# Optimization experiments

Hardware: AMD Instinct MI355X
Metric: run time of the kernel (lower is better)

The kernel has to match this reference:

```python
import jax, jax.numpy as jnp
import numpy as np

EPS = 1e-5

def group_norm(x, num_groups, eps=EPS):
    # x: [B, C, H, W]; no affine (matches F.group_norm with weight=None)
    B, C, H, W = x.shape
    xg = x.reshape(B, num_groups, (C // num_groups) * H * W)
    mean = jnp.mean(xg, axis=-1, keepdims=True)
    var = jnp.var(xg, axis=-1, keepdims=True)
    xg = (xg - mean) * jax.lax.rsqrt(var + eps)
    return xg.reshape(B, C, H, W)

def setup_inputs() -> dict:
    key = jax.random.key(0)
    ks = jax.random.split(key, 5)
    B, C, H, W = 32, 256, 32, 32
    # kaiming-uniform-ish scale for linear weights
    bound = 1.0 / np.sqrt(C)
    x = jax.random.normal(ks[0], (B, C, H, W), dtype=jnp.float32)
    WQ = jax.random.uniform(ks[1], (C, C), jnp.float32, -bound, bound)
    WK = jax.random.uniform(ks[2], (C, C), jnp.float32, -bound, bound)
    WV = jax.random.uniform(ks[3], (C, C), jnp.float32, -bound, bound)
    Wo = jax.random.uniform(ks[4], (C, C), jnp.float32, -bound, bound)
    z = jnp.zeros((C,), jnp.float32)
    return {"x": x, "WQ": WQ, "bQ": z, "WK": WK, "bK": z,
            "WV": WV, "bV": z, "Wo": Wo, "bo": z}

def reference(x, WQ, bQ, WK, bK, WV, bV, Wo, bo):
    B, C, H, W = x.shape
    G = min(32, C)
    h = group_norm(x, G)                      # [B,C,H,W]
    h = h.reshape(B, C, H * W).transpose(0, 2, 1)  # [B, S, C], S = H*W
    q = h @ WQ + bQ
    k = h @ WK + bK
    v = h @ WV + bV
    scale = C ** (-0.5)
    attn = jnp.einsum('bsc,btc->bst', q, k) * scale   # [B,S,S]
    attn = jax.nn.softmax(attn, axis=-1)
    o = jnp.einsum('bst,btc->bsc', attn, v)           # [B,S,C]
    o = o @ Wo + bo                                   # output Nin while in [B,S,C]
    o = o.transpose(0, 2, 1).reshape(B, C, H, W)
    return x + o
```

## Files before the change

### kernel.cpp

```cpp
#include <hip/hip_runtime.h>
#include <stdint.h>

#define BB  32
#define CC  256
#define SS  1024
#define GG  32
#define GCH 8
#define EPS 1e-5f

typedef __attribute__((ext_vector_type(8))) short short8;
typedef __attribute__((ext_vector_type(4))) float f32x4;
typedef __attribute__((ext_vector_type(16))) float f32x16;
typedef unsigned short ushort;

__device__ __forceinline__ float bf2f(ushort u){
  union { unsigned int i; float f; } v; v.i = ((unsigned int)u) << 16; return v.f;
}
__device__ __forceinline__ ushort f2bf(float f){
  union { float f; unsigned int i; } v; v.f = f;
  unsigned int r = v.i + 0x7FFFu + ((v.i >> 16) & 1u);
  return (ushort)(r >> 16);
}

typedef __attribute__((address_space(3))) unsigned int lds_uint;
typedef const __attribute__((address_space(1))) unsigned int glob_uint;
__device__ __forceinline__ void ld_lds16(const void* g, void* l){
  __builtin_amdgcn_global_load_lds((glob_uint*)g, (lds_uint*)l, 16, 0, 0);
}

__global__ __launch_bounds__(256) void sniff_k(const unsigned int* __restrict__ xw,
                                               int* __restrict__ flag)
{
  const int tid = threadIdx.x;
  unsigned int w = xw[tid];
  ushort lo = (ushort)(w & 0xFFFFu);
  int e = (lo >> 7) & 0xFF;
  int ok = (lo == 0 || (e >= 100 && e <= 130)) ? 1 : 0;
  __shared__ int cnt;
  if (tid == 0) cnt = 0;
  __syncthreads();
  atomicAdd(&cnt, ok);
  __syncthreads();
  if (tid == 0) *flag = (cnt > 192) ? 1 : 0;
}

__global__ __launch_bounds__(256) void convert_pre(
    const void* w0, const void* w1, const void* w2, const void* w3,
    const void* b0, const void* b1, const void* b2, const void* b3,
    ushort* __restrict__ WT, float* __restrict__ biasF,
    const int* __restrict__ flag)
{
  const int f = *flag;
  const int z = blockIdx.z;
  const float scl = (z == 0) ? 0.0625f : 1.0f;
  const void* wsel = z==0?w0:z==1?w1:z==2?w2:w3;
  ushort* dst = WT + (long long)z * 65536;
  __shared__ ushort t[64][65];
  const int tid = threadIdx.x;
  const int tx = tid & 63, ty = tid >> 6;
  const int r0 = blockIdx.x * 64, c0 = blockIdx.y * 64;
  for (int j = 0; j < 64; j += 4){
    const int idx = (r0+ty+j)*256 + c0+tx;
    float v = f ? bf2f(((const ushort*)wsel)[idx]) : ((const float*)wsel)[idx];
    t[ty+j][tx] = f2bf(v * scl);
  }
  __syncthreads();
  for (int j = 0; j < 64; j += 4) dst[(c0+ty+j)*256 + r0+tx] = t[tx][ty+j];
  if (blockIdx.x == 0 && blockIdx.y == 0){
    const void* bsel = z==0?b0:z==1?b1:z==2?b2:b3;
    float bv = f ? bf2f(((const ushort*)bsel)[tid]) : ((const float*)bsel)[tid];
    biasF[z*256 + tid] = bv * scl;
  }
}

__global__ __launch_bounds__(256) void gn_stats(const void* __restrict__ x,
                                                float* __restrict__ stats,
                                                const int* __restrict__ flag)
{
  const int f = *flag;
  const int g = blockIdx.x, b = blockIdx.y;
  const int tid = threadIdx.x;
  const long long base = ((long long)b * CC + g * GCH) * SS;
  float sum = 0.f, ss = 0.f;
  if (f){
    const ushort* xg = (const ushort*)x + base;
    #pragma unroll
    for (int j = 0; j < 4; j++){
      uint4 u = *(const uint4*)(xg + (j*256 + tid)*8);
      const ushort* e = (const ushort*)&u;
      #pragma unroll
      for (int i = 0; i < 8; i++){ float v = bf2f(e[i]); sum += v; ss += v*v; }
    }
  } else {
    const float* xg = (const float*)x + base;
    #pragma unroll
    for (int j = 0; j < 8; j++){
      float4 v4 = *(const float4*)(xg + (j*256 + tid)*4);
      sum += v4.x+v4.y+v4.z+v4.w;
      ss  += v4.x*v4.x+v4.y*v4.y+v4.z*v4.z+v4.w*v4.w;
    }
  }
  __shared__ float red[8];
  const int lane = tid & 63, w = tid >> 6;
  #pragma unroll
  for (int o = 32; o > 0; o >>= 1){
    sum += __shfl_down(sum, o);
    ss  += __shfl_down(ss, o);
  }
  if (lane == 0){ red[w] = sum; red[4+w] = ss; }
  __syncthreads();
  if (tid == 0){
    float s1 = red[0]+red[1]+red[2]+red[3];
    float s2 = red[4]+red[5]+red[6]+red[7];
    float mean = s1 / (float)(GCH*SS);
    float var  = s2 / (float)(GCH*SS) - mean*mean;
    const int idx = b*GG + g;
    stats[idx*2]   = mean;
    stats[idx*2+1] = rsqrtf(var + EPS);
  }
}

__global__ __launch_bounds__(256) void gn_norm(const void* __restrict__ x,
                                               ushort* __restrict__ h,
                                               const float* __restrict__ stats,
                                               const int* __restrict__ flag)
{
  const int f = *flag;
  const int c0 = blockIdx.x * 64, s0 = blockIdx.y * 64, b = blockIdx.z;
  const int tid = threadIdx.x;
  __shared__ ushort T[64][72];
  const int row = tid >> 2;
  const int qr  = tid & 3;
  const int g = (c0 + row) >> 3;
  const float mean = stats[(b*GG + g)*2];
  const float rstd = stats[(b*GG + g)*2 + 1];
  const long long xrow = ((long long)b * CC + c0 + row) * SS + s0;
  if (f){
    const ushort* xr = (const ushort*)x + xrow;
    #pragma unroll
    for (int j = 0; j < 2; j++){
      const int col = qr*16 + j*8;
      uint4 u = *(const uint4*)(xr + col);
      const ushort* e = (const ushort*)&u;
      #pragma unroll
      for (int i = 0; i < 8; i++) T[row][col+i] = f2bf((bf2f(e[i]) - mean) * rstd);
    }
  } else {
    const float* xr = (const float*)x + xrow;
    #pragma unroll
    for (int j = 0; j < 4; j++){
      const int col = qr*16 + j*4;
      float4 v4 = *(const float4*)(xr + col);
      T[row][col+0] = f2bf((v4.x - mean) * rstd);
      T[row][col+1] = f2bf((v4.y - mean) * rstd);
      T[row][col+2] = f2bf((v4.z - mean) * rstd);
      T[row][col+3] = f2bf((v4.w - mean) * rstd);
    }
  }
  __syncthreads();
  #pragma unroll
  for (int pass = 0; pass < 2; pass++){
    const int sr = pass*32 + (tid >> 3);
    const int cl = (tid & 7) * 8;
    ushort tmp[8];
    #pragma unroll
    for (int e = 0; e < 8; e++) tmp[e] = T[cl+e][sr];
    *(uint4*)(&h[((long long)b * SS + s0 + sr) * CC + c0 + cl]) = *(const uint4*)tmp;
  }
}

template<int MODE>
__global__ __launch_bounds__(256) void gemm128(
    const ushort* __restrict__ A,
    const ushort* __restrict__ BT,
    ushort* __restrict__ Cmat,
    int lda, int ldb, int ldc, int K,
    long long sA, long long sB, long long sC,
    const float* __restrict__ biasF,
    const void* __restrict__ xres,
    void* __restrict__ outp,
    ushort* __restrict__ vTp,
    long long xoff,
    const int* __restrict__ flag)
{
  extern __shared__ __attribute__((aligned(16))) ushort smem[];
  ushort* As = smem;
  ushort* Bs = smem + 5120;
  const int tid  = threadIdx.x;
  const int lane = tid & 63;
  const int w    = tid >> 6;
  const int wr   = w >> 1, wc = w & 1;
  const int bz   = blockIdx.z;
  const int m0 = blockIdx.x * 128;
  const int n0 = blockIdx.y * 128;

  const int srow  = tid >> 1;
  const int shalf = (tid & 1) * 16;

  f32x4 acc[4][4] = {};

  const ushort* Ablk = A + (long long)bz * sA + (long long)(m0 + srow) * lda + shalf;
  const ushort* Bblk = BT + (long long)bz * sB + (long long)(n0 + srow) * ldb + shalf;
  ushort* asw = &As[srow * 40 + shalf];
  ushort* bsw = &Bs[srow * 40 + shalf];

  const int koff = 8 * (lane >> 4);
  const int rr   = lane & 15;

  for (int k0 = 0; k0 < K; k0 += 32){
    uint4 va0 = *(const uint4*)(Ablk + k0);
    uint4 va1 = *(const uint4*)(Ablk + k0 + 8);
    uint4 vb0 = *(const uint4*)(Bblk + k0);
    uint4 vb1 = *(const uint4*)(Bblk + k0 + 8);
    *(uint4*)(asw)     = va0;
    *(uint4*)(asw + 8) = va1;
    *(uint4*)(bsw)     = vb0;
    *(uint4*)(bsw + 8) = vb1;
    __syncthreads();
    short8 af[4], bfr[4];
    #pragma unroll
    for (int mf = 0; mf < 4; mf++)
      af[mf] = *(const short8*)(&As[(wr*64 + mf*16 + rr) * 40 + koff]);
    #pragma unroll
    for (int nf = 0; nf < 4; nf++)
      bfr[nf] = *(const short8*)(&Bs[(wc*64 + nf*16 + rr) * 40 + koff]);
    #pragma unroll
    for (int mf = 0; mf < 4; mf++)
      #pragma unroll
      for (int nf = 0; nf < 4; nf++)
        acc[mf][nf] = __builtin_amdgcn_mfma_f32_16x16x32_bf16(af[mf], bfr[nf], acc[mf][nf], 0, 0, 0);
    __syncthreads();
  }

  const int rb = 4 * (lane >> 4);
  if (MODE == 0){
    if (bz < 2){
      ushort* Co = Cmat + (long long)bz * sC;
      #pragma unroll
      for (int mf = 0; mf < 4; mf++){
        #pragma unroll
        for (int nf = 0; nf < 4; nf++){
          const int col = n0 + wc*64 + nf*16 + rr;
          const float badd = biasF[bz*256 + col];
          #pragma unroll
          for (int r = 0; r < 4; r++){
            const int row = m0 + wr*64 + mf*16 + rb + r;
            Co[(long long)row * ldc + col] = f2bf(acc[mf][nf][r] + badd);
          }
        }
      }
    } else {
      #pragma unroll
      for (int mf = 0; mf < 4; mf++){
        #pragma unroll
        for (int nf = 0; nf < 4; nf++){
          const int col = n0 + wc*64 + nf*16 + rr;
          const float badd = biasF[512 + col];
          #pragma unroll
          for (int r = 0; r < 4; r++){
            const int row = m0 + wr*64 + mf*16 + rb + r;
            const int bL = row >> 10, s = row & 1023;
            vTp[((long long)bL * CC + col) * SS + s] = f2bf(acc[mf][nf][r] + badd);
          }
        }
      }
    }
  } else {
    const int bL = m0 >> 10;
    const int s0 = m0 & 1023;
    #pragma unroll
    for (int mf = 0; mf < 4; mf++){
      #pragma unroll
      for (int nf = 0; nf < 4; nf++){
        const int colL = wc*64 + nf*16 + rr;
        const float badd = biasF[768 + n0 + colL];
        #pragma unroll
        for (int r = 0; r < 4; r++){
          const int rowL = wr*64 + mf*16 + rb + r;
          smem[colL * 128 + rowL] = f2bf(acc[mf][nf][r] + badd);
        }
      }
    }
    __syncthreads();
    const int f = *flag;
    for (int i = tid; i < 2048; i += 256){
      const int colL = i >> 4;
      const int rowL = (i & 15) * 8;
      const long long oi = xoff + ((long long)bL * CC + n0 + colL) * SS + s0 + rowL;
      const ushort* pu = &smem[colL * 128 + rowL];
      if (f){
        const ushort* xu = (const ushort*)xres + oi;
        ushort* ou = (ushort*)outp + oi;
        ushort tmp[8];
        #pragma unroll
        for (int e = 0; e < 8; e++) tmp[e] = f2bf(bf2f(xu[e]) + bf2f(pu[e]));
        *(uint4*)ou = *(const uint4*)tmp;
      } else {
        const float* xf = (const float*)xres + oi;
        float* of = (float*)outp + oi;
        float4 a0 = *(const float4*)xf;
        float4 a1 = *(const float4*)(xf + 4);
        float4 r0, r1;
        r0.x = a0.x + bf2f(pu[0]); r0.y = a0.y + bf2f(pu[1]);
        r0.z = a0.z + bf2f(pu[2]); r0.w = a0.w + bf2f(pu[3]);
        r1.x = a1.x + bf2f(pu[4]); r1.y = a1.y + bf2f(pu[5]);
        r1.z = a1.z + bf2f(pu[6]); r1.w = a1.w + bf2f(pu[7]);
        *(float4*)of = r0;
        *(float4*)(of + 4) = r1;
      }
    }
  }
}

__global__ __launch_bounds__(512, 1) void attn_fused(
    const ushort* __restrict__ q, const ushort* __restrict__ k,
    const ushort* __restrict__ vT, ushort* __restrict__ oC)
{
  __shared__ ushort Kb[2][64 * 256];
  __shared__ ushort Vb[2][256 * 64];
  const int tid = threadIdx.x, lane = tid & 63, w = tid >> 6;
  const int l31 = lane & 31, hi2 = lane >> 5;
  const int qg = w & 3, ch = w >> 2;
  const int b = blockIdx.x, qt = blockIdx.y;

  const char* kgB = (const char*)(k + (long long)b * SS * CC);
  const char* vgB = (const char*)(vT + (long long)b * CC * SS);
  const int qrow = qt*128 + qg*32 + l31;
  const ushort* qgp = q + ((long long)b * SS + qrow) * CC + hi2*8;
  ushort* ogq = oC + ((long long)b * SS + qrow) * CC + ch*128;

  short8 qf[16];
  #pragma unroll
  for (int kk = 0; kk < 16; kk++)
    qf[kk] = *(const short8*)(qgp + kk*16);

  f32x16 Oa[4] = {};
  float mrow = -1e30f, lrow = 0.0f;

  #define STAGE(buf, t0)                                                        \
  {                                                                             \
    _Pragma("unroll")                                                           \
    for (int j = 0; j < 4; j++){                                                \
      const int ck = j*8 + w;                                                   \
      const int tr = ck*2 + (lane >> 5);                                        \
      const int xb = ((lane & 31) * 16) ^ ((tr & 31) << 4);                     \
      ld_lds16(kgB + (long long)((t0) + tr) * 512 + xb, &Kb[buf][ck * 512]);    \
    }                                                                           \
    _Pragma("unroll")                                                           \
    for (int j = 0; j < 4; j++){                                                \
      const int ck = j*8 + w;                                                   \
      const int cr = ck*8 + (lane >> 3);                                        \
      const int yb = ((lane & 7) * 16) ^ ((cr & 7) << 4);                       \
      ld_lds16(vgB + (long long)cr * 2048 + (t0)*2 + yb, &Vb[buf][ck * 512]);   \
    }                                                                           \
  }

  STAGE(0, 0);
  asm volatile("s_waitcnt vmcnt(0)" ::: "memory");
  __builtin_amdgcn_sched_barrier(0);
  __syncthreads();

  const int coff = hi2 * 16;
  const int kswz = l31 << 4;

  for (int t = 0; t < 16; t++){
    const int cur = t & 1;
    if (t < 15) STAGE(cur ^ 1, (t+1)*64);

    f32x16 Sa0 = {}, Sa1 = {};
    __builtin_amdgcn_s_setprio(1);
    #pragma unroll
    for (int kk = 0; kk < 16; kk++){
      const int off = kk*32 + coff;
      short8 ka0 = *(const short8*)((const char*)&Kb[cur][0] + l31*512 + (off ^ kswz));
      short8 ka1 = *(const short8*)((const char*)&Kb[cur][0] + (32 + l31)*512 + (off ^ kswz));
      Sa0 = __builtin_amdgcn_mfma_f32_32x32x16_bf16(ka0, qf[kk], Sa0, 0, 0, 0);
      Sa1 = __builtin_amdgcn_mfma_f32_32x32x16_bf16(ka1, qf[kk], Sa1, 0, 0, 0);
    }
    __builtin_amdgcn_s_setprio(0);

    float mx = Sa0[0];
    #pragma unroll
    for (int r = 1; r < 16; r++) mx = fmaxf(mx, Sa0[r]);
    #pragma unroll
    for (int r = 0; r < 16; r++) mx = fmaxf(mx, Sa1[r]);
    mx = fmaxf(mx, __shfl_xor(mx, 32));
    if (!__all(mx <= mrow)){
      const float mn = fmaxf(mrow, mx);
      const float sc = __expf(mrow - mn);
      mrow = mn;
      lrow *= sc;
      #pragma unroll
      for (int nf = 0; nf < 4; nf++)
        #pragma unroll
        for (int r = 0; r < 16; r++) Oa[nf][r] *= sc;
    }
    float rs = 0.0f;
    #pragma unroll
    for (int r = 0; r < 16; r++){
      Sa0[r] = __expf(Sa0[r] - mrow); rs += Sa0[r];
      Sa1[r] = __expf(Sa1[r] - mrow); rs += Sa1[r];
    }
    rs += __shfl_xor(rs, 32);
    lrow += rs;

    __builtin_amdgcn_s_setprio(1);
    #pragma unroll
    for (int g = 0; g < 4; g++){
      float pv[8];
      #pragma unroll
      for (int j = 0; j < 8; j++)
        pv[j] = (g < 2) ? Sa0[(g & 1)*8 + j] : Sa1[(g & 1)*8 + j];
      unsigned int b0 = ((unsigned int)f2bf(pv[1]) << 16) | f2bf(pv[0]);
      unsigned int b1 = ((unsigned int)f2bf(pv[3]) << 16) | f2bf(pv[2]);
      unsigned int b2 = ((unsigned int)f2bf(pv[5]) << 16) | f2bf(pv[4]);
      unsigned int b3 = ((unsigned int)f2bf(pv[7]) << 16) | f2bf(pv[6]);
      unsigned int s0 = (unsigned int)__shfl_xor((int)b0, 32);
      unsigned int s1 = (unsigned int)__shfl_xor((int)b1, 32);
      unsigned int s2 = (unsigned int)__shfl_xor((int)b2, 32);
      unsigned int s3 = (unsigned int)__shfl_xor((int)b3, 32);
      union { uint4 u; short8 s; } pw;
      pw.u.x = hi2 ? s2 : b0;
      pw.u.y = hi2 ? s3 : b1;
      pw.u.z = hi2 ? b2 : s0;
      pw.u.w = hi2 ? b3 : s1;
      const short8 pb = pw.s;
      const int voff = g*32 + coff;
      #pragma unroll
      for (int nf = 0; nf < 4; nf++){
        const int c = ch*128 + nf*32 + l31;
        short8 va = *(const short8*)((const char*)&Vb[cur][0] + c*128 + (voff ^ ((c & 7) << 4)));
        Oa[nf] = __builtin_amdgcn_mfma_f32_32x32x16_bf16(va, pb, Oa[nf], 0, 0, 0);
      }
    }
    __builtin_amdgcn_s_setprio(0);

    asm volatile("s_waitcnt vmcnt(0)" ::: "memory");
    __builtin_amdgcn_sched_barrier(0);
    __syncthreads();
  }
  #undef STAGE

  const float inv = 1.0f / lrow;
  #pragma unroll
  for (int nf = 0; nf < 4; nf++){
    #pragma unroll
    for (int g = 0; g < 4; g++){
      ushort t4[4];
      #pragma unroll
      for (int j = 0; j < 4; j++) t4[j] = f2bf(Oa[nf][g*4 + j] * inv);
      *(uint2*)(ogq + nf*32 + g*8 + hi2*4) = *(const uint2*)t4;
    }
  }
}

extern "C" void kernel_launch(void* const* d_in, const int* in_sizes, int n_in,
                              void* d_out, int out_size, void* d_ws, size_t ws_size,
                              hipStream_t stream)
{
  (void)in_sizes; (void)n_in; (void)out_size;
  const void* x  = d_in[0];
  const void* WQ = d_in[1];
  const void* bQ = d_in[2];
  const void* WK = d_in[3];
  const void* bK = d_in[4];
  const void* WV = d_in[5];
  const void* bV = d_in[6];
  const void* Wo = d_in[7];
  const void* bo = d_in[8];

  const long long NE  = (long long)BB * SS * CC;
  const long long SC  = (long long)SS * CC;

  uint8_t* base = (uint8_t*)d_ws;
  int* flag          = (int*)base;
  float* biasF       = (float*)(base + 256);
  float* stats       = (float*)(base + 256 + 4096);
  ushort* WT         = (ushort*)(base + 256 + 4096 + 8192);
  ushort* h          = WT + 4 * 65536;

  const long long fixedB = 256 + 4096 + 8192 + 4LL*65536*2 + NE*2;
  int CB = 1;
  for (int c = 32; c >= 1; c >>= 1){
    if (fixedB + 4LL * c * SC * 2 <= (long long)ws_size){ CB = c; break; }
  }

  ushort* q  = h + NE;
  ushort* k  = q + (long long)CB * SC;
  ushort* vT = k + (long long)CB * SC;
  ushort* oC = vT + (long long)CB * SC;

  dim3 blk(256);
  const size_t shmem = 32768;

  sniff_k<<<1, blk, 0, stream>>>((const unsigned int*)x, flag);
  convert_pre<<<dim3(4, 4, 4), blk, 0, stream>>>(WQ, WK, WV, Wo, bQ, bK, bV, bo, WT, biasF, flag);
  gn_stats<<<dim3(GG, BB), blk, 0, stream>>>(x, stats, flag);
  gn_norm<<<dim3(4, 16, BB), blk, 0, stream>>>(x, h, stats, flag);

  for (int c0 = 0; c0 < BB; c0 += CB){
    const ushort* hC = h + (long long)c0 * SC;
    gemm128<0><<<dim3(CB*8, 2, 3), blk, shmem, stream>>>(
        hC, WT, q, CC, CC, CC, CC,
        0LL, 65536LL, (long long)CB * SC,
        biasF, nullptr, nullptr, vT, 0LL, flag);
    attn_fused<<<dim3(CB, 8), dim3(512), 0, stream>>>(q, k, vT, oC);
    gemm128<3><<<dim3(CB*8, 2, 1), blk, shmem, stream>>>(
        oC, WT + 3*65536, nullptr, CC, CC, SS, CC,
        0LL, 0LL, 0LL,
        biasF, x, d_out, nullptr, (long long)c0 * SC, flag);
  }
}
```

Before: 163.0 us.

## Use exp2 softmax with folded log2e, lazy rescale, packed bf16 converts, new V swizzle

Folds log2(e) into the Q weight scale so the softmax can use the native exp2 instruction instead of __expf. It also skips rescaling the running max unless the new max exceeds the old by more than 8, and replaces manual bf16 rounding with the hardware v_cvt_pk_bf16_f32 instruction. Separately, it changes the V tile LDS layout and swizzle, likely to cut bank conflicts on the PV MFMA operand loads. The lazy rescale trades some headroom against overflow of the exponentials for fewer rescale passes over the accumulators.

```diff
diff --git a/kernel.cpp b/kernel.cpp
--- a/kernel.cpp
+++ b/kernel.cpp
@@ -20,6 +20,11 @@
   union { float f; unsigned int i; } v; v.f = f;
   unsigned int r = v.i + 0x7FFFu + ((v.i >> 16) & 1u);
   return (ushort)(r >> 16);
+}
+__device__ __forceinline__ unsigned int cvt_pk_bf16(float lo, float hi){
+  unsigned int r;
+  asm("v_cvt_pk_bf16_f32 %0, %1, %2" : "=v"(r) : "v"(lo), "v"(hi));
+  return r;
 }
 
 typedef __attribute__((address_space(3))) unsigned int lds_uint;
@@ -52,7 +57,7 @@
 {
   const int f = *flag;
   const int z = blockIdx.z;
-  const float scl = (z == 0) ? 0.0625f : 1.0f;
+  const float scl = (z == 0) ? 0.0901684400557f : 1.0f;
   const void* wsel = z==0?w0:z==1?w1:z==2?w2:w3;
   ushort* dst = WT + (long long)z * 65536;
   __shared__ ushort t[64][65];
@@ -349,9 +354,11 @@
     _Pragma("unroll")                                                           \
     for (int j = 0; j < 4; j++){                                                \
       const int ck = j*8 + w;                                                   \
-      const int cr = ck*8 + (lane >> 3);                                        \
-      const int yb = ((lane & 7) * 16) ^ ((cr & 7) << 4);                       \
-      ld_lds16(vgB + (long long)cr * 2048 + (t0)*2 + yb, &Vb[buf][ck * 512]);   \
+      const int vr = ck*2 + (lane >> 5);                                        \
+      const int u  = (lane & 31) ^ ((vr & 7) << 2);                             \
+      const int vc = vr*4 + (u & 3);                                            \
+      const int tb = (u >> 2) * 16;                                             \
+      ld_lds16(vgB + (long long)vc * 2048 + (t0)*2 + tb, &Vb[buf][ck * 512]);   \
     }                                                                           \
   }
 
@@ -385,9 +392,9 @@
     #pragma unroll
     for (int r = 0; r < 16; r++) mx = fmaxf(mx, Sa1[r]);
     mx = fmaxf(mx, __shfl_xor(mx, 32));
-    if (!__all(mx <= mrow)){
+    if (!__all(mx <= mrow + 8.0f)){
       const float mn = fmaxf(mrow, mx);
-      const float sc = __expf(mrow - mn);
+      const float sc = __builtin_amdgcn_exp2f(mrow - mn);
       mrow = mn;
       lrow *= sc;
       #pragma unroll
@@ -398,8 +405,8 @@
     float rs = 0.0f;
     #pragma unroll
     for (int r = 0; r < 16; r++){
-      Sa0[r] = __expf(Sa0[r] - mrow); rs += Sa0[r];
-      Sa1[r] = __expf(Sa1[r] - mrow); rs += Sa1[r];
+      Sa0[r] = __builtin_amdgcn_exp2f(Sa0[r] - mrow); rs += Sa0[r];
+      Sa1[r] = __builtin_amdgcn_exp2f(Sa1[r] - mrow); rs += Sa1[r];
     }
     rs += __shfl_xor(rs, 32);
     lrow += rs;
@@ -407,14 +414,18 @@
     __builtin_amdgcn_s_setprio(1);
     #pragma unroll
     for (int g = 0; g < 4; g++){
-      float pv[8];
-      #pragma unroll
-      for (int j = 0; j < 8; j++)
-        pv[j] = (g < 2) ? Sa0[(g & 1)*8 + j] : Sa1[(g & 1)*8 + j];
-      unsigned int b0 = ((unsigned int)f2bf(pv[1]) << 16) | f2bf(pv[0]);
-      unsigned int b1 = ((unsigned int)f2bf(pv[3]) << 16) | f2bf(pv[2]);
-      unsigned int b2 = ((unsigned int)f2bf(pv[5]) << 16) | f2bf(pv[4]);
-      unsigned int b3 = ((unsigned int)f2bf(pv[7]) << 16) | f2bf(pv[6]);
+      unsigned int b0, b1, b2, b3;
+      if (g < 2){
+        b0 = cvt_pk_bf16(Sa0[(g&1)*8+0], Sa0[(g&1)*8+1]);
+        b1 = cvt_pk_bf16(Sa0[(g&1)*8+2], Sa0[(g&1)*8+3]);
+        b2 = cvt_pk_bf16(Sa0[(g&1)*8+4], Sa0[(g&1)*8+5]);
+        b3 = cvt_pk_bf16(Sa0[(g&1)*8+6], Sa0[(g&1)*8+7]);
+      } else {
+        b0 = cvt_pk_bf16(Sa1[(g&1)*8+0], Sa1[(g&1)*8+1]);
+        b1 = cvt_pk_bf16(Sa1[(g&1)*8+2], Sa1[(g&1)*8+3]);
+        b2 = cvt_pk_bf16(Sa1[(g&1)*8+4], Sa1[(g&1)*8+5]);
+        b3 = cvt_pk_bf16(Sa1[(g&1)*8+6], Sa1[(g&1)*8+7]);
+      }
       unsigned int s0 = (unsigned int)__shfl_xor((int)b0, 32);
       unsigned int s1 = (unsigned int)__shfl_xor((int)b1, 32);
       unsigned int s2 = (unsigned int)__shfl_xor((int)b2, 32);
@@ -425,11 +436,13 @@
       pw.u.z = hi2 ? b2 : s0;
       pw.u.w = hi2 ? b3 : s1;
       const short8 pb = pw.s;
-      const int voff = g*32 + coff;
+      const int G = g*2 + hi2;
       #pragma unroll
       for (int nf = 0; nf < 4; nf++){
         const int c = ch*128 + nf*32 + l31;
-        short8 va = *(const short8*)((const char*)&Vb[cur][0] + c*128 + (voff ^ ((c & 7) << 4)));
+        const int vr = c >> 2;
+        const int slot = (((G << 2) | (c & 3)) ^ ((vr & 7) << 2));
+        short8 va = *(const short8*)((const char*)&Vb[cur][0] + vr*512 + slot*16);
         Oa[nf] = __builtin_amdgcn_mfma_f32_32x32x16_bf16(va, pb, Oa[nf], 0, 0, 0);
       }
     }
@@ -446,10 +459,10 @@
   for (int nf = 0; nf < 4; nf++){
     #pragma unroll
     for (int g = 0; g < 4; g++){
-      ushort t4[4];
-      #pragma unroll
-      for (int j = 0; j < 4; j++) t4[j] = f2bf(Oa[nf][g*4 + j] * inv);
-      *(uint2*)(ogq + nf*32 + g*8 + hi2*4) = *(const uint2*)t4;
+      uint2 ov;
+      ov.x = cvt_pk_bf16(Oa[nf][g*4+0] * inv, Oa[nf][g*4+1] * inv);
+      ov.y = cvt_pk_bf16(Oa[nf][g*4+2] * inv, Oa[nf][g*4+3] * inv);
+      *(uint2*)(ogq + nf*32 + g*8 + hi2*4) = ov;
     }
   }
 }
```

After: 157.8 us. -3.2%, faster.
